# Optimization experiments

Hardware: AMD Instinct MI355X
Metric: run time of the kernel (lower is better)

## Reference

```python
import jax, jax.numpy as jnp
import numpy as np


def setup_inputs() -> dict:
    key = jax.random.key(0)
    kq, kk, kv = jax.random.split(key, 3)
    B, H, S, D = 4, 16, 2048, 64
    Q = jax.random.normal(kq, (B, H, S, D), dtype=jnp.float32)
    K = jax.random.normal(kk, (B, H, S, D), dtype=jnp.float32)
    V = jax.random.normal(kv, (B, H, S, D), dtype=jnp.float32)
    return {"Q": Q, "K": K, "V": V}


def reference(Q, K, V):
    # Faithful to the source: scale = d**(-2); scores = (Q @ K^T) / scale
    # i.e. scores are MULTIPLIED by d^2 (quirk of the original module).
    d = K.shape[-1]
    scale = jnp.asarray(d, Q.dtype) ** (-2)
    scores = jnp.einsum('bhqd,bhkd->bhqk', Q, K) / scale  # [B,H,S,S]
    attn = jax.nn.softmax(scores, axis=-1)
    out = jnp.einsum('bhqk,bhkd->bhqd', attn, V)
    return out
```

## Files before the change

kernel.cpp:

```cpp
#include <hip/hip_runtime.h>
#include <math.h>


#define S_LEN 2048
#define D_DIM 64
#define NH 64
#define BM 128
#define BN 32
#define QTILES (S_LEN / BM)
#define KTILES (S_LEN / BN)

typedef unsigned short u16;
typedef unsigned int u32;
typedef _Float16 f16;
typedef __attribute__((ext_vector_type(8))) _Float16 f16x8;
typedef __attribute__((ext_vector_type(2))) __fp16 fp16x2;
typedef __attribute__((ext_vector_type(4))) float f32x4;

#define SC_FULL (4096.0f * 1.4426950408889634f)
#define QSCALE (SC_FULL / 64.0f)
#define KSCALE 64.0f

union f16cv { f16 h; u16 u; };
union pkcv { fp16x2 h; u32 u; };

__device__ __forceinline__ void split2h(float a, u16& hi, u16& lo) {
  f16cv ch, cl;
  ch.h = (f16)a;
  float r = a - (float)ch.h;
  cl.h = (f16)r;
  hi = ch.u; lo = cl.u;
}

__global__ void prep_kernel(const float* __restrict__ K, const float* __restrict__ V,
                            u16* __restrict__ Kh, u16* __restrict__ Km,
                            u16* __restrict__ Vt) {
  if (blockIdx.x < 8192) {
    size_t i4 = ((size_t)blockIdx.x * 256 + threadIdx.x) * 4;
    float4 v = *(const float4*)(K + i4);
    u16 h0, l0, h1, l1, h2, l2, h3, l3;
    split2h(v.x * KSCALE, h0, l0);
    split2h(v.y * KSCALE, h1, l1);
    split2h(v.z * KSCALE, h2, l2);
    split2h(v.w * KSCALE, h3, l3);
    *(uint2*)(Kh + i4) = make_uint2((u32)h0 | ((u32)h1 << 16), (u32)h2 | ((u32)h3 << 16));
    *(uint2*)(Km + i4) = make_uint2((u32)l0 | ((u32)l1 << 16), (u32)l2 | ((u32)l3 << 16));
  } else {
    __shared__ float Vf[64 * 65];
    const int idx = blockIdx.x - 8192;
    const int kt = idx & 31, h = idx >> 5;
    const int tid = threadIdx.x;
    const float* V0 = V + ((size_t)h * S_LEN + kt * 64) * 64;
    const int tx = tid & 15, ty = tid >> 4;
#pragma unroll
    for (int p = 0; p < 4; ++p) {
      int r = ty + 16 * p;
      float4 v = *(const float4*)(V0 + r * 64 + tx * 4);
      Vf[r * 65 + 4 * tx + 0] = v.x;
      Vf[r * 65 + 4 * tx + 1] = v.y;
      Vf[r * 65 + 4 * tx + 2] = v.z;
      Vf[r * 65 + 4 * tx + 3] = v.w;
    }
    __syncthreads();
    const int ch = tid & 7, dr = tid >> 3;
#pragma unroll
    for (int p = 0; p < 2; ++p) {
      int d = dr + 32 * p;
      u32 w[4];
#pragma unroll
      for (int i = 0; i < 4; ++i) {
        f16cv a, b;
        a.h = (f16)Vf[(8 * ch + 2 * i) * 65 + d];
        b.h = (f16)Vf[(8 * ch + 2 * i + 1) * 65 + d];
        w[i] = (u32)a.u | ((u32)b.u << 16);
      }
      size_t o = ((size_t)h * 64 + d) * S_LEN + (size_t)kt * 64 + 8 * ch;
      *(uint4*)(Vt + o) = make_uint4(w[0], w[1], w[2], w[3]);
    }
  }
}

#define BUF_USH 6144
#define P_B 12288
#define LDS_USH 16384

__device__ __forceinline__ void gld16(const u16* g, u16* l) {
  __builtin_amdgcn_global_load_lds(
      (const __attribute__((address_space(1))) void*)g,
      (__attribute__((address_space(3))) void*)l, 16, 0, 0);
}

__global__ __launch_bounds__(256, 4)
void attn_mfma_f16(const float* __restrict__ Q, const u16* __restrict__ Kh,
                   const u16* __restrict__ Km, const u16* __restrict__ Vt,
                   float* __restrict__ O) {
  __shared__ __align__(16) u16 lds[LDS_USH];

  const int tid = threadIdx.x;
  const int lane = tid & 63;
  const int wv = tid >> 6;
  const int c = lane & 15;
  const int g = lane >> 4;
  const int h = blockIdx.x;
  const int qtile = blockIdx.y;

  f16x8 aqh[2][2], aqm[2][2];
#pragma unroll
  for (int m = 0; m < 2; ++m) {
    int qrow = qtile * BM + wv * 32 + m * 16 + c;
    const float* qp = Q + ((size_t)h * S_LEN + qrow) * 64 + g * 8;
#pragma unroll
    for (int ks = 0; ks < 2; ++ks) {
      float4 a = *(const float4*)(qp + ks * 32);
      float4 b = *(const float4*)(qp + ks * 32 + 4);
      float v[8] = {a.x, a.y, a.z, a.w, b.x, b.y, b.z, b.w};
      f16x8 hi, lo;
#pragma unroll
      for (int e = 0; e < 8; ++e) {
        float q = v[e] * QSCALE;
        f16 qh = (f16)q;
        hi[e] = qh;
        lo[e] = (f16)(q - (float)qh);
      }
      aqh[m][ks] = hi; aqm[m][ks] = lo;
    }
  }

  f32x4 Oacc[2][4];
  float mrow[2] = {-INFINITY, -INFINITY};
  float lrow[2] = {0.f, 0.f};
#pragma unroll
  for (int m = 0; m < 2; ++m)
#pragma unroll
    for (int t = 0; t < 4; ++t) Oacc[m][t] = (f32x4){0.f, 0.f, 0.f, 0.f};

  const int rowK = tid >> 3;
  const int chK  = (tid & 7) ^ (rowK & 7);
  const int rowV = tid >> 2;
  const int chV  = (tid & 3) ^ (rowV & 3);
  const u16* kh_src = Kh + (size_t)h * (S_LEN * 64) + rowK * 64 + chK * 8;
  const u16* km_src = Km + (size_t)h * (S_LEN * 64) + rowK * 64 + chK * 8;
  const u16* vt_src = Vt + ((size_t)h * 64 + rowV) * S_LEN + chV * 8;
  const int ldsW = wv * 512;

  gld16(kh_src, lds + 0    + ldsW);
  gld16(km_src, lds + 2048 + ldsW);
  gld16(vt_src, lds + 4096 + ldsW);

#pragma unroll 2
  for (int kt = 0; kt < KTILES; ++kt) {
    const int bo = (kt & 1) * BUF_USH;
    __syncthreads();

    if (kt + 1 < KTILES) {
      const int bn = ((kt + 1) & 1) * BUF_USH;
      gld16(kh_src + (size_t)(kt + 1) * 2048, lds + bn + 0    + ldsW);
      gld16(km_src + (size_t)(kt + 1) * 2048, lds + bn + 2048 + ldsW);
      gld16(vt_src + (size_t)(kt + 1) * 32,   lds + bn + 4096 + ldsW);
    }

    f32x4 S[2][2];
#pragma unroll
    for (int m = 0; m < 2; ++m)
#pragma unroll
      for (int t = 0; t < 2; ++t) S[m][t] = (f32x4){0.f, 0.f, 0.f, 0.f};
    __builtin_amdgcn_s_setprio(1);
#pragma unroll
    for (int ks = 0; ks < 2; ++ks) {
#pragma unroll
      for (int t = 0; t < 2; ++t) {
        int rk = 16 * t + c;
        int off = bo + rk * 64 + (((g + 4 * ks) ^ (rk & 7)) << 3);
        f16x8 bh = *(const f16x8*)&lds[off];
        f16x8 bm = *(const f16x8*)&lds[off + 2048];
#pragma unroll
        for (int m = 0; m < 2; ++m) {
          S[m][t] = __builtin_amdgcn_mfma_f32_16x16x32_f16(bh, aqh[m][ks], S[m][t], 0, 0, 0);
          S[m][t] = __builtin_amdgcn_mfma_f32_16x16x32_f16(bm, aqh[m][ks], S[m][t], 0, 0, 0);
          S[m][t] = __builtin_amdgcn_mfma_f32_16x16x32_f16(bh, aqm[m][ks], S[m][t], 0, 0, 0);
        }
      }
    }
    __builtin_amdgcn_s_setprio(0);

#pragma unroll
    for (int m = 0; m < 2; ++m) {
      float x0 = fmaxf(S[m][0][0], S[m][0][1]);
      float x1 = fmaxf(S[m][0][2], S[m][0][3]);
      float x2 = fmaxf(S[m][1][0], S[m][1][1]);
      float x3 = fmaxf(S[m][1][2], S[m][1][3]);
      float mx = fmaxf(fmaxf(x0, x1), fmaxf(x2, x3));
      mx = fmaxf(mx, __shfl_xor(mx, 16));
      mx = fmaxf(mx, __shfl_xor(mx, 32));
      float mnew = fmaxf(mrow[m], mx);
      float a = exp2f(mrow[m] - mnew);
      mrow[m] = mnew;
      float ps = 0.f;
#pragma unroll
      for (int t = 0; t < 2; ++t)
#pragma unroll
        for (int r = 0; r < 4; ++r) {
          float p = exp2f(S[m][t][r] - mnew);
          S[m][t][r] = p;
          ps += p;
        }
      lrow[m] = lrow[m] * a + ps;
      if (a < 1.0f) {
#pragma unroll
        for (int nt = 0; nt < 4; ++nt)
#pragma unroll
          for (int r = 0; r < 4; ++r) Oacc[m][nt][r] *= a;
      }
      int rql = wv * 32 + m * 16 + c;
      int rbase = P_B + (rql << 5);
      int rs3 = rql & 3;
#pragma unroll
      for (int t = 0; t < 2; ++t) {
        pkcv p01, p23;
        p01.h = __builtin_amdgcn_cvt_pkrtz(S[m][t][0], S[m][t][1]);
        p23.h = __builtin_amdgcn_cvt_pkrtz(S[m][t][2], S[m][t][3]);
        int off = rbase + (((2 * t + (g >> 1)) ^ rs3) << 3) + 4 * (g & 1);
        *(uint2*)&lds[off] = make_uint2(p01.u, p23.u);
      }
    }

    f16x8 ap[2];
#pragma unroll
    for (int m = 0; m < 2; ++m) {
      int rql = wv * 32 + m * 16 + c;
      ap[m] = *(const f16x8*)&lds[P_B + (rql << 5) + ((g ^ (rql & 3)) << 3)];
    }
    __builtin_amdgcn_s_setprio(1);
#pragma unroll
    for (int nt = 0; nt < 4; ++nt) {
      int rv = 16 * nt + c;
      f16x8 bv = *(const f16x8*)&lds[bo + 4096 + (rv << 5) + ((g ^ (rv & 3)) << 3)];
#pragma unroll
      for (int m = 0; m < 2; ++m)
        Oacc[m][nt] = __builtin_amdgcn_mfma_f32_16x16x32_f16(bv, ap[m], Oacc[m][nt], 0, 0, 0);
    }
    __builtin_amdgcn_s_setprio(0);
  }

#pragma unroll
  for (int m = 0; m < 2; ++m) {
    float l = lrow[m];
    l += __shfl_xor(l, 16);
    l += __shfl_xor(l, 32);
    float linv = 1.0f / l;
    int q = qtile * BM + wv * 32 + m * 16 + c;
    float* op = O + ((size_t)h * S_LEN + q) * 64 + 4 * g;
#pragma unroll
    for (int nt = 0; nt < 4; ++nt) {
      float4 o;
      o.x = Oacc[m][nt][0] * linv;
      o.y = Oacc[m][nt][1] * linv;
      o.z = Oacc[m][nt][2] * linv;
      o.w = Oacc[m][nt][3] * linv;
      *(float4*)(op + 16 * nt) = o;
    }
  }
}

#define LSTR 68
__global__ __launch_bounds__(256, 2)
void attn_fp32_kernel(const float* __restrict__ Q, const float* __restrict__ K,
                      const float* __restrict__ V, float* __restrict__ O) {
  __shared__ float Qs[64][LSTR];
  __shared__ float Ks[64][LSTR];
  __shared__ float Vs[64][LSTR];
  __shared__ float Ps[64][LSTR];
  const int tid = threadIdx.x;
  const int tx = tid & 15, ty = tid >> 4;
  const int qtile = blockIdx.x, head = blockIdx.y;
  const long hoff = (long)head * S_LEN * D_DIM;
  const float* Qp = Q + hoff + (long)qtile * 64 * D_DIM;
  const float* Kp = K + hoff;
  const float* Vp = V + hoff;
  float* Op = O + hoff + (long)qtile * 64 * D_DIM;
  {
    const int cc = tx * 4;
#pragma unroll
    for (int p = 0; p < 4; ++p) {
      const int r = ty + p * 16;
      *(float4*)(&Qs[r][cc]) = *(const float4*)(Qp + r * D_DIM + cc);
    }
  }
  float m_i[4], l_i[4];
  float4 o_acc[4];
#pragma unroll
  for (int i = 0; i < 4; ++i) {
    m_i[i] = -INFINITY; l_i[i] = 0.0f;
    o_acc[i] = make_float4(0.f, 0.f, 0.f, 0.f);
  }
  const float SCALE = 4096.0f;
  const float LOG2E = 1.4426950408889634f;
  for (int kt = 0; kt < S_LEN / 64; ++kt) {
    {
      const int cc = tx * 4;
      const float* Kt = Kp + kt * 64 * D_DIM;
      const float* Vv = Vp + kt * 64 * D_DIM;
#pragma unroll
      for (int p = 0; p < 4; ++p) {
        const int r = ty + p * 16;
        *(float4*)(&Ks[r][cc]) = *(const float4*)(Kt + r * D_DIM + cc);
        *(float4*)(&Vs[r][cc]) = *(const float4*)(Vv + r * D_DIM + cc);
      }
    }
    __syncthreads();
    float s[4][4];
#pragma unroll
    for (int i = 0; i < 4; ++i)
#pragma unroll
      for (int j = 0; j < 4; ++j) s[i][j] = 0.0f;
#pragma unroll
    for (int d = 0; d < D_DIM; d += 4) {
      float4 q4[4], k4[4];
#pragma unroll
      for (int i = 0; i < 4; ++i) q4[i] = *(const float4*)(&Qs[ty * 4 + i][d]);
#pragma unroll
      for (int j = 0; j < 4; ++j) k4[j] = *(const float4*)(&Ks[tx + 16 * j][d]);
#pragma unroll
      for (int i = 0; i < 4; ++i)
#pragma unroll
        for (int j = 0; j < 4; ++j) {
          s[i][j] += q4[i].x * k4[j].x; s[i][j] += q4[i].y * k4[j].y;
          s[i][j] += q4[i].z * k4[j].z; s[i][j] += q4[i].w * k4[j].w;
        }
    }
#pragma unroll
    for (int i = 0; i < 4; ++i) {
#pragma unroll
      for (int j = 0; j < 4; ++j) s[i][j] *= SCALE;
      float rm = fmaxf(fmaxf(s[i][0], s[i][1]), fmaxf(s[i][2], s[i][3]));
#pragma unroll
      for (int off = 8; off >= 1; off >>= 1) rm = fmaxf(rm, __shfl_xor(rm, off));
      const float mnew = fmaxf(m_i[i], rm);
      const float alpha = exp2f((m_i[i] - mnew) * LOG2E);
      float rs = 0.0f;
#pragma unroll
      for (int j = 0; j < 4; ++j) {
        const float p = exp2f((s[i][j] - mnew) * LOG2E);
        s[i][j] = p; rs += p;
      }
#pragma unroll
      for (int off = 8; off >= 1; off >>= 1) rs += __shfl_xor(rs, off);
      l_i[i] = l_i[i] * alpha + rs;
      m_i[i] = mnew;
      o_acc[i].x *= alpha; o_acc[i].y *= alpha; o_acc[i].z *= alpha; o_acc[i].w *= alpha;
      const int mm = ty * 4 + i;
      Ps[mm][tx] = s[i][0]; Ps[mm][tx + 16] = s[i][1];
      Ps[mm][tx + 32] = s[i][2]; Ps[mm][tx + 48] = s[i][3];
    }
    __syncthreads();
#pragma unroll
    for (int k = 0; k < 64; k += 4) {
      float4 p4[4], v4[4];
#pragma unroll
      for (int i = 0; i < 4; ++i) p4[i] = *(const float4*)(&Ps[ty * 4 + i][k]);
#pragma unroll
      for (int kk = 0; kk < 4; ++kk) v4[kk] = *(const float4*)(&Vs[k + kk][tx * 4]);
#pragma unroll
      for (int i = 0; i < 4; ++i) {
        o_acc[i].x += p4[i].x * v4[0].x + p4[i].y * v4[1].x + p4[i].z * v4[2].x + p4[i].w * v4[3].x;
        o_acc[i].y += p4[i].x * v4[0].y + p4[i].y * v4[1].y + p4[i].z * v4[2].y + p4[i].w * v4[3].y;
        o_acc[i].z += p4[i].x * v4[0].z + p4[i].y * v4[1].z + p4[i].z * v4[2].z + p4[i].w * v4[3].z;
        o_acc[i].w += p4[i].x * v4[0].w + p4[i].y * v4[1].w + p4[i].z * v4[2].w + p4[i].w * v4[3].w;
      }
    }
    __syncthreads();
  }
#pragma unroll
  for (int i = 0; i < 4; ++i) {
    const float inv = 1.0f / l_i[i];
    o_acc[i].x *= inv; o_acc[i].y *= inv; o_acc[i].z *= inv; o_acc[i].w *= inv;
    *(float4*)(Op + (ty * 4 + i) * D_DIM + tx * 4) = o_acc[i];
  }
}

extern "C" void kernel_launch(void* const* d_in, const int* in_sizes, int n_in,
                              void* d_out, int out_size, void* d_ws, size_t ws_size,
                              hipStream_t stream) {
  const float* Q = (const float*)d_in[0];
  const float* K = (const float*)d_in[1];
  const float* V = (const float*)d_in[2];
  float* O = (float*)d_out;

  const size_t P = (size_t)NH * S_LEN * D_DIM;
  const size_t need = 3 * P * sizeof(u16);

  if (ws_size >= need) {
    u16* w = (u16*)d_ws;
    u16 *Kh = w, *Km = w + P, *Vt = w + 2 * P;
    prep_kernel<<<8192 + 2048, 256, 0, stream>>>(K, V, Kh, Km, Vt);
    attn_mfma_f16<<<dim3(NH, QTILES), 256, 0, stream>>>(Q, Kh, Km, Vt, O);
  } else {
    attn_fp32_kernel<<<dim3(S_LEN / 64, NH), 256, 0, stream>>>(Q, K, V, O);
  }
}
```

Measured before the change: 333.7 us.

## Restructure attention loop: BN=64, register P via 16x16x16 MFMA, deferred PV, lazy rescale

Doubles the key tile to 64 and keeps the softmax probabilities in registers as f16x4 fragments that feed 16x16x16 MFMAs directly, so P no longer round-trips through LDS. The PV product for a tile is deferred into the next iteration, letting it overlap with that tile's QK work. K is single-buffered with a second barrier, while V stays double-buffered. Row-max rescaling is skipped unless the new max exceeds the old one by more than 8 in log2 units, which saves multiplies but risks f16 overflow headroom in P. The 16x16x16 MFMA also has half the K-depth per instruction, so the PV step issues more instructions.

```diff
diff --git a/kernel.cpp b/kernel.cpp
--- a/kernel.cpp
+++ b/kernel.cpp
@@ -6,13 +6,14 @@
 #define D_DIM 64
 #define NH 64
 #define BM 128
-#define BN 32
+#define BN 64
 #define QTILES (S_LEN / BM)
 #define KTILES (S_LEN / BN)
 
 typedef unsigned short u16;
 typedef unsigned int u32;
 typedef _Float16 f16;
+typedef __attribute__((ext_vector_type(4))) _Float16 f16x4;
 typedef __attribute__((ext_vector_type(8))) _Float16 f16x8;
 typedef __attribute__((ext_vector_type(2))) __fp16 fp16x2;
 typedef __attribute__((ext_vector_type(4))) float f32x4;
@@ -23,6 +24,7 @@
 
 union f16cv { f16 h; u16 u; };
 union pkcv { fp16x2 h; u32 u; };
+union pk4 { fp16x2 h2[2]; f16x4 v; };
 
 __device__ __forceinline__ void split2h(float a, u16& hi, u16& lo) {
   f16cv ch, cl;
@@ -80,8 +82,9 @@
   }
 }
 
-#define BUF_USH 6144
-#define P_B 12288
+#define K0_B 0
+#define K1_B 4096
+#define VT_B 8192
 #define LDS_USH 16384
 
 __device__ __forceinline__ void gld16(const u16* g, u16* l) {
@@ -90,7 +93,8 @@
       (__attribute__((address_space(3))) void*)l, 16, 0, 0);
 }
 
-__global__ __launch_bounds__(256, 4)
+__global__ __launch_bounds__(256)
+__attribute__((amdgpu_waves_per_eu(4, 4)))
 void attn_mfma_f16(const float* __restrict__ Q, const u16* __restrict__ Kh,
                    const u16* __restrict__ Km, const u16* __restrict__ Vt,
                    float* __restrict__ O) {
@@ -104,6 +108,20 @@
   const int h = blockIdx.x;
   const int qtile = blockIdx.y;
 
+  const int r5 = tid >> 3;
+  const int ch = (tid & 7) ^ (r5 & 7);
+  const u16* kh0 = Kh + (size_t)h * (S_LEN * 64) + r5 * 64 + ch * 8;
+  const u16* km0 = Km + (size_t)h * (S_LEN * 64) + r5 * 64 + ch * 8;
+  const u16* vt0 = Vt + ((size_t)h * 64 + r5) * S_LEN + ch * 8;
+  const int ldsW = wv * 512;
+
+#pragma unroll
+  for (int p = 0; p < 2; ++p) {
+    gld16(kh0 + p * 2048, lds + K0_B + p * 2048 + ldsW);
+    gld16(km0 + p * 2048, lds + K1_B + p * 2048 + ldsW);
+    gld16(vt0 + (size_t)p * (32 * S_LEN), lds + VT_B + p * 2048 + ldsW);
+  }
+
   f16x8 aqh[2][2], aqm[2][2];
 #pragma unroll
   for (int m = 0; m < 2; ++m) {
@@ -134,45 +152,47 @@
 #pragma unroll
     for (int t = 0; t < 4; ++t) Oacc[m][t] = (f32x4){0.f, 0.f, 0.f, 0.f};
 
-  const int rowK = tid >> 3;
-  const int chK  = (tid & 7) ^ (rowK & 7);
-  const int rowV = tid >> 2;
-  const int chV  = (tid & 3) ^ (rowV & 3);
-  const u16* kh_src = Kh + (size_t)h * (S_LEN * 64) + rowK * 64 + chK * 8;
-  const u16* km_src = Km + (size_t)h * (S_LEN * 64) + rowK * 64 + chK * 8;
-  const u16* vt_src = Vt + ((size_t)h * 64 + rowV) * S_LEN + chV * 8;
-  const int ldsW = wv * 512;
-
-  gld16(kh_src, lds + 0    + ldsW);
-  gld16(km_src, lds + 2048 + ldsW);
-  gld16(vt_src, lds + 4096 + ldsW);
+  f16x4 ap[2][4];
+
+  auto pv_step = [&](int vbuf) {
+    const int vbase = VT_B + vbuf * 4096;
+    __builtin_amdgcn_s_setprio(1);
+#pragma unroll
+    for (int nt = 0; nt < 4; ++nt) {
+      const int rv = 16 * nt + c;
+      const int rb = vbase + rv * 64 + 4 * (g & 1);
+      const int r7 = rv & 7;
+#pragma unroll
+      for (int t = 0; t < 4; ++t) {
+        f16x4 bv = *(const f16x4*)&lds[rb + (((2 * t + (g >> 1)) ^ r7) << 3)];
+#pragma unroll
+        for (int m = 0; m < 2; ++m)
+          Oacc[m][nt] = __builtin_amdgcn_mfma_f32_16x16x16f16(bv, ap[m][t], Oacc[m][nt], 0, 0, 0);
+      }
+    }
+    __builtin_amdgcn_s_setprio(0);
+  };
 
 #pragma unroll 2
   for (int kt = 0; kt < KTILES; ++kt) {
-    const int bo = (kt & 1) * BUF_USH;
-    __syncthreads();
-
-    if (kt + 1 < KTILES) {
-      const int bn = ((kt + 1) & 1) * BUF_USH;
-      gld16(kh_src + (size_t)(kt + 1) * 2048, lds + bn + 0    + ldsW);
-      gld16(km_src + (size_t)(kt + 1) * 2048, lds + bn + 2048 + ldsW);
-      gld16(vt_src + (size_t)(kt + 1) * 32,   lds + bn + 4096 + ldsW);
-    }
-
-    f32x4 S[2][2];
+    __syncthreads();
+
+    if (kt > 0) pv_step((kt - 1) & 1);
+
+    f32x4 S[2][4];
 #pragma unroll
     for (int m = 0; m < 2; ++m)
 #pragma unroll
-      for (int t = 0; t < 2; ++t) S[m][t] = (f32x4){0.f, 0.f, 0.f, 0.f};
+      for (int t = 0; t < 4; ++t) S[m][t] = (f32x4){0.f, 0.f, 0.f, 0.f};
     __builtin_amdgcn_s_setprio(1);
 #pragma unroll
     for (int ks = 0; ks < 2; ++ks) {
 #pragma unroll
-      for (int t = 0; t < 2; ++t) {
+      for (int t = 0; t < 4; ++t) {
         int rk = 16 * t + c;
-        int off = bo + rk * 64 + (((g + 4 * ks) ^ (rk & 7)) << 3);
-        f16x8 bh = *(const f16x8*)&lds[off];
-        f16x8 bm = *(const f16x8*)&lds[off + 2048];
+        int off = rk * 64 + (((g + 4 * ks) ^ (rk & 7)) << 3);
+        f16x8 bh = *(const f16x8*)&lds[K0_B + off];
+        f16x8 bm = *(const f16x8*)&lds[K1_B + off];
 #pragma unroll
         for (int m = 0; m < 2; ++m) {
           S[m][t] = __builtin_amdgcn_mfma_f32_16x16x32_f16(bh, aqh[m][ks], S[m][t], 0, 0, 0);
@@ -183,64 +203,56 @@
     }
     __builtin_amdgcn_s_setprio(0);
 
+    __syncthreads();
+
+    if (kt + 1 < KTILES) {
+      const int vn = (kt + 1) & 1;
+#pragma unroll
+      for (int p = 0; p < 2; ++p) {
+        gld16(kh0 + (size_t)(kt + 1) * 4096 + p * 2048, lds + K0_B + p * 2048 + ldsW);
+        gld16(km0 + (size_t)(kt + 1) * 4096 + p * 2048, lds + K1_B + p * 2048 + ldsW);
+        gld16(vt0 + (size_t)(kt + 1) * 64 + (size_t)p * (32 * S_LEN),
+              lds + VT_B + vn * 4096 + p * 2048 + ldsW);
+      }
+    }
+
 #pragma unroll
     for (int m = 0; m < 2; ++m) {
-      float x0 = fmaxf(S[m][0][0], S[m][0][1]);
-      float x1 = fmaxf(S[m][0][2], S[m][0][3]);
-      float x2 = fmaxf(S[m][1][0], S[m][1][1]);
-      float x3 = fmaxf(S[m][1][2], S[m][1][3]);
+      float x0 = fmaxf(fmaxf(S[m][0][0], S[m][0][1]), fmaxf(S[m][0][2], S[m][0][3]));
+      float x1 = fmaxf(fmaxf(S[m][1][0], S[m][1][1]), fmaxf(S[m][1][2], S[m][1][3]));
+      float x2 = fmaxf(fmaxf(S[m][2][0], S[m][2][1]), fmaxf(S[m][2][2], S[m][2][3]));
+      float x3 = fmaxf(fmaxf(S[m][3][0], S[m][3][1]), fmaxf(S[m][3][2], S[m][3][3]));
       float mx = fmaxf(fmaxf(x0, x1), fmaxf(x2, x3));
       mx = fmaxf(mx, __shfl_xor(mx, 16));
       mx = fmaxf(mx, __shfl_xor(mx, 32));
-      float mnew = fmaxf(mrow[m], mx);
-      float a = exp2f(mrow[m] - mnew);
-      mrow[m] = mnew;
+      if (!__all(mx - mrow[m] <= 8.0f)) {
+        float mnew = fmaxf(mrow[m], mx);
+        float a = exp2f(mrow[m] - mnew);
+        mrow[m] = mnew;
+        lrow[m] *= a;
+#pragma unroll
+        for (int nt = 0; nt < 4; ++nt)
+#pragma unroll
+          for (int r = 0; r < 4; ++r) Oacc[m][nt][r] *= a;
+      }
       float ps = 0.f;
 #pragma unroll
-      for (int t = 0; t < 2; ++t)
-#pragma unroll
-        for (int r = 0; r < 4; ++r) {
-          float p = exp2f(S[m][t][r] - mnew);
-          S[m][t][r] = p;
-          ps += p;
-        }
-      lrow[m] = lrow[m] * a + ps;
-      if (a < 1.0f) {
-#pragma unroll
-        for (int nt = 0; nt < 4; ++nt)
-#pragma unroll
-          for (int r = 0; r < 4; ++r) Oacc[m][nt][r] *= a;
-      }
-      int rql = wv * 32 + m * 16 + c;
-      int rbase = P_B + (rql << 5);
-      int rs3 = rql & 3;
-#pragma unroll
-      for (int t = 0; t < 2; ++t) {
-        pkcv p01, p23;
-        p01.h = __builtin_amdgcn_cvt_pkrtz(S[m][t][0], S[m][t][1]);
-        p23.h = __builtin_amdgcn_cvt_pkrtz(S[m][t][2], S[m][t][3]);
-        int off = rbase + (((2 * t + (g >> 1)) ^ rs3) << 3) + 4 * (g & 1);
-        *(uint2*)&lds[off] = make_uint2(p01.u, p23.u);
-      }
-    }
-
-    f16x8 ap[2];
-#pragma unroll
-    for (int m = 0; m < 2; ++m) {
-      int rql = wv * 32 + m * 16 + c;
-      ap[m] = *(const f16x8*)&lds[P_B + (rql << 5) + ((g ^ (rql & 3)) << 3)];
-    }
-    __builtin_amdgcn_s_setprio(1);
-#pragma unroll
-    for (int nt = 0; nt < 4; ++nt) {
-      int rv = 16 * nt + c;
-      f16x8 bv = *(const f16x8*)&lds[bo + 4096 + (rv << 5) + ((g ^ (rv & 3)) << 3)];
-#pragma unroll
-      for (int m = 0; m < 2; ++m)
-        Oacc[m][nt] = __builtin_amdgcn_mfma_f32_16x16x32_f16(bv, ap[m], Oacc[m][nt], 0, 0, 0);
-    }
-    __builtin_amdgcn_s_setprio(0);
-  }
+      for (int t = 0; t < 4; ++t) {
+        float p0 = exp2f(S[m][t][0] - mrow[m]);
+        float p1 = exp2f(S[m][t][1] - mrow[m]);
+        float p2 = exp2f(S[m][t][2] - mrow[m]);
+        float p3 = exp2f(S[m][t][3] - mrow[m]);
+        ps += (p0 + p1) + (p2 + p3);
+        pk4 w;
+        w.h2[0] = __builtin_amdgcn_cvt_pkrtz(p0, p1);
+        w.h2[1] = __builtin_amdgcn_cvt_pkrtz(p2, p3);
+        ap[m][t] = w.v;
+      }
+      lrow[m] += ps;
+    }
+  }
+
+  pv_step((KTILES - 1) & 1);
 
 #pragma unroll
   for (int m = 0; m < 2; ++m) {
```

After: 522.4 us. 1.57x slower.
